# Kernel tuning notes

Measured on AMD Instinct MI355X. Metric: run time of the kernel, lower is better.

Reference implementation:

```python
import jax, jax.numpy as jnp
import numpy as np

B, C, H, W, NH = 4, 96, 256, 256, 4


def setup_inputs() -> dict:
    key = jax.random.key(0)
    ks = jax.random.split(key, 8)
    s = 0.05  # keep pre-activations well-scaled
    return {
        "x": jax.random.normal(ks[0], (B, C, H, W), jnp.float32),
        "ff": jax.random.normal(ks[1], (B, C, H, W), jnp.float32),
        "w_q": jax.random.normal(ks[2], (C, C, 1, 1), jnp.float32) * s,
        "w_kv": jax.random.normal(ks[3], (2 * C, C, 1, 1), jnp.float32) * s,
        "w_q_dw": jax.random.normal(ks[4], (C, 1, 3, 3), jnp.float32) * s,
        "w_kv_dw": jax.random.normal(ks[5], (2 * C, 1, 3, 3), jnp.float32) * s,
        "w_out": jax.random.normal(ks[6], (C, C, 1, 1), jnp.float32) * s,
        "temperature": jnp.ones((NH, 1, 1), jnp.float32),
    }


def _conv1x1(x, w):
    # pointwise conv == channel GEMM; w: [O, I, 1, 1]
    return jnp.einsum('bchw,oc->bohw', x, w[:, :, 0, 0])


def _dwconv3(x, w):
    # depthwise 3x3, padding=1; w: [C, 1, 3, 3]
    return jax.lax.conv_general_dilated(
        x, w, window_strides=(1, 1), padding='SAME',
        feature_group_count=x.shape[1],
        dimension_numbers=('NCHW', 'OIHW', 'NCHW'))


def _l2norm(t, eps=1e-12):
    # L2-normalize along last (HW) axis, torch F.normalize semantics
    n = jnp.sqrt(jnp.sum(t * t, axis=-1, keepdims=True))
    return t / jnp.maximum(n, eps)


def reference(x, ff, w_q, w_kv, w_q_dw, w_kv_dw, w_out, temperature):
    b, c, h, w = x.shape
    q = _dwconv3(_conv1x1(ff, w_q), w_q_dw)          # [B,C,H,W]
    kv = _dwconv3(_conv1x1(x, w_kv), w_kv_dw)        # [B,2C,H,W]
    k, v = jnp.split(kv, 2, axis=1)

    def heads(t):
        return t.reshape(b, NH, c // NH, h * w)       # [B,nh,c,HW]

    q = _l2norm(heads(q))
    k = _l2norm(heads(k))
    v = heads(v)
    # channel-wise (transposed) attention: [B,nh,c,c]
    attn = jax.nn.softmax(jnp.einsum('bhcn,bhdn->bhcd', q, k) * temperature, axis=-1)
    o = jnp.einsum('bhcd,bhdn->bhcn', attn, v).reshape(b, c, h, w)
    return _conv1x1(o, w_out)
```

## Files before the change

### kernel.cpp

```cpp
#include <hip/hip_runtime.h>
#include <hip/hip_bf16.h>
#include <hip/hip_fp16.h>

typedef unsigned int u32;
typedef unsigned short u16;
typedef _Float16 f16;

static constexpr int HWn = 65536;

typedef __attribute__((ext_vector_type(8))) f16 f16x8;
typedef __attribute__((ext_vector_type(2))) f16 f16x2;
typedef __attribute__((ext_vector_type(4))) float f32x4;

__device__ __forceinline__ float h2f(u16 u) {
    union { u16 s; f16 h; } z; z.s = u; return (float)z.h;
}
__device__ __forceinline__ u16 f2h(float f) {
    union { u16 s; f16 h; } z; z.h = (f16)f; return z.s;
}
__device__ __forceinline__ u32 pack2h(float a, float b) {
    union { u32 i; f16 h[2]; } z; z.h[0] = (f16)a; z.h[1] = (f16)b; return z.i;
}
__device__ __forceinline__ float hlo(u32 u) {
    union { u32 i; f16 h[2]; } z; z.i = u; return (float)z.h[0];
}
__device__ __forceinline__ float hhi(u32 u) {
    union { u32 i; f16 h[2]; } z; z.i = u; return (float)z.h[1];
}
__device__ __forceinline__ float sq2h(u32 a) {
    const float l = hlo(a), h = hhi(a);
    return fmaf(l, l, h * h);
}

#if defined(__has_builtin)
#if __has_builtin(__builtin_amdgcn_fdot2)
#define HAS_FDOT2 1
#endif
#endif
__device__ __forceinline__ float fdot2a(u32 a, u32 b, float c) {
#ifdef HAS_FDOT2
    union { u32 i; f16x2 h; } A, B; A.i = a; B.i = b;
    return __builtin_amdgcn_fdot2(A.h, B.h, c, false);
#else
    return fmaf(hlo(a), hlo(b), fmaf(hhi(a), hhi(b), c));
#endif
}

__device__ __forceinline__ int xoff(int px, int icb) {
    return px * 128 + (((icb ^ (px & 7) ^ ((px >> 3) & 7))) << 3);
}

__global__ __launch_bounds__(256) void k_prep_w(
    const float* __restrict__ wq, const float* __restrict__ wkv,
    u16* __restrict__ wf)
{
    const int i = blockIdx.x * 256 + threadIdx.x;
    if (i >= 288 * 96) return;
    const int row = i / 96, ic = i % 96;
    const float w = (row < 96) ? wq[row * 96 + ic] : wkv[(row - 96) * 96 + ic];
    wf[i] = f2h(w);
}

__global__ __launch_bounds__(256, 3) void k_conv_mfma(
    const float* __restrict__ ff, const float* __restrict__ x,
    const u16* __restrict__ wf,
    u16* __restrict__ qpre, u16* __restrict__ kvpre)
{
    const int b = blockIdx.z, sec = blockIdx.y;
    const int pxb = blockIdx.x * 256;
    const int tid = threadIdx.x;

    __shared__ __align__(16) u16 xs[16384];

    const float* src = (sec == 0 ? ff : x) + (size_t)b * 96 * HWn;
    const int icq = (tid >> 4) * 2;
    const int pxs = (tid & 15) * 8;
    const int lane = tid & 63;
    const int wv = tid >> 6;
    const int oc0 = (wv >> 1) * 48;
    const int pxw = (wv & 1) * 64;
    const int lr = lane & 15, lg = lane >> 4;

    float4 L[12];

    auto issue = [&](int px0) {
        #pragma unroll
        for (int p = 0; p < 3; ++p) {
            const float* rp0 = src + (size_t)(p * 32 + icq) * HWn + px0 + pxs;
            const float* rp1 = rp0 + HWn;
            L[p * 4 + 0] = *reinterpret_cast<const float4*>(rp0);
            L[p * 4 + 1] = *reinterpret_cast<const float4*>(rp0 + 4);
            L[p * 4 + 2] = *reinterpret_cast<const float4*>(rp1);
            L[p * 4 + 3] = *reinterpret_cast<const float4*>(rp1 + 4);
        }
    };
    auto stage = [&]() {
        #pragma unroll
        for (int p = 0; p < 3; ++p) {
            const int ic = p * 32 + icq;
            const int icb = ic >> 3, icl = ic & 7;
            const float e0[8] = {L[p*4+0].x, L[p*4+0].y, L[p*4+0].z, L[p*4+0].w,
                                 L[p*4+1].x, L[p*4+1].y, L[p*4+1].z, L[p*4+1].w};
            const float e1[8] = {L[p*4+2].x, L[p*4+2].y, L[p*4+2].z, L[p*4+2].w,
                                 L[p*4+3].x, L[p*4+3].y, L[p*4+3].z, L[p*4+3].w};
            #pragma unroll
            for (int j = 0; j < 8; ++j) {
                const int o = xoff(pxs + j, icb) + icl;
                *reinterpret_cast<u32*>(&xs[o]) = pack2h(e0[j], e1[j]);
            }
        }
    };
    auto compute = [&](int px0) {
        const int npass = (sec == 0) ? 1 : 2;
        #pragma unroll 1
        for (int kvs = 0; kvs < npass; ++kvs) {
            const u16* wh = wf + ((sec == 0) ? 0 : (96 + kvs * 96)) * 96;
            u16* dst = (sec == 0) ? (qpre + (size_t)b * 96 * HWn)
                                  : (kvpre + (size_t)b * 192 * HWn + (size_t)kvs * 96 * HWn);
            f32x4 acc[4][3];
            #pragma unroll
            for (int n = 0; n < 4; ++n)
                #pragma unroll
                for (int m = 0; m < 3; ++m)
                    acc[n][m] = (f32x4){0.f, 0.f, 0.f, 0.f};

            #pragma unroll 1
            for (int kt = 0; kt < 3; ++kt) {
                const int kb = kt * 32;
                f16x8 XA[4];
                #pragma unroll
                for (int n = 0; n < 4; ++n)
                    XA[n] = *(const f16x8*)(xs + xoff(pxw + n * 16 + lr, (kb >> 3) + lg));
                f16x8 WB[3];
                #pragma unroll
                for (int m = 0; m < 3; ++m)
                    WB[m] = *(const f16x8*)(wh + (oc0 + m * 16 + lr) * 96 + kb + lg * 8);
                #pragma unroll
                for (int n = 0; n < 4; ++n)
                    #pragma unroll
                    for (int m = 0; m < 3; ++m)
                        acc[n][m] = __builtin_amdgcn_mfma_f32_16x16x32_f16(XA[n], WB[m], acc[n][m], 0, 0, 0);
            }

            #pragma unroll
            for (int n = 0; n < 4; ++n) {
                #pragma unroll
                for (int m = 0; m < 3; ++m) {
                    const int oc = oc0 + m * 16 + lr;
                    ushort4 sv;
                    sv.x = f2h(acc[n][m][0]); sv.y = f2h(acc[n][m][1]);
                    sv.z = f2h(acc[n][m][2]); sv.w = f2h(acc[n][m][3]);
                    *reinterpret_cast<ushort4*>(dst + (size_t)oc * HWn + px0 + pxw + n * 16 + lg * 4) = sv;
                }
            }
        }
    };

    issue(pxb);
    stage();
    __syncthreads();
    issue(pxb + 128);
    compute(pxb);
    __syncthreads();
    stage();
    __syncthreads();
    compute(pxb + 128);
}

__device__ __forceinline__ void row3tap(
    const uint4 m, u32 lv, u32 rv, u32 w01, u32 w2z, float* a)
{
    const u32 P0 = m.x, P1 = m.y, P2 = m.z, P3 = m.w;
    const u32 s0 = (lv >> 16) | (P0 << 16);
    const u32 s1 = (P0 >> 16) | (P1 << 16);
    const u32 s2 = (P1 >> 16) | (P2 << 16);
    const u32 s3 = (P2 >> 16) | (P3 << 16);
    const u32 s4 = (P3 >> 16) | (rv << 16);
    a[0] = fdot2a(w2z, s1, fdot2a(w01, s0, a[0]));
    a[1] = fdot2a(w2z, P1, fdot2a(w01, P0, a[1]));
    a[2] = fdot2a(w2z, s2, fdot2a(w01, s1, a[2]));
    a[3] = fdot2a(w2z, P2, fdot2a(w01, P1, a[3]));
    a[4] = fdot2a(w2z, s3, fdot2a(w01, s2, a[4]));
    a[5] = fdot2a(w2z, P3, fdot2a(w01, P2, a[5]));
    a[6] = fdot2a(w2z, s4, fdot2a(w01, s3, a[6]));
    a[7] = fdot2a(w2z, rv, fdot2a(w01, P3, a[7]));
}

__global__ __launch_bounds__(512) void k_dw_qk(
    const u16* __restrict__ qpre, const u16* __restrict__ kvpre,
    const float* __restrict__ wqdw, const float* __restrict__ wkvdw,
    float* __restrict__ ssq, float* __restrict__ Sg)
{
    const int bid = blockIdx.x;
    const int wg = (bid & 7) * 256 + (bid >> 3);
    const int b = wg >> 9;
    const int rem = wg & 511;
    const int y = rem >> 1;
    const int tx = (rem & 1) * 128;
    const int tid = threadIdx.x;
    const int lane = tid & 63;
    const int pq = tid >> 4;
    const int chunk = tid & 15;
    const int x0l = chunk * 8;
    const int xg = tx + x0l;

    const bool vr0 = (y > 0), vr2 = (y < 255);
    const bool le = (chunk == 0) && (xg > 0);
    const bool re = (chunk == 15) && (xg + 8 < 256);

    __shared__ __align__(16) u16 qs[96][136];
    __shared__ __align__(16) u16 ks[96][136];

    auto addr = [&](int it, const u16*& src, const float*& wp, int& c, int& seg) {
        const int p = it * 32 + pq;
        if (p < 96) { c = p;      src = qpre  + ((size_t)(b * 96 + c)) * HWn;  wp = wqdw  + c * 9; seg = 0; }
        else        { c = p - 96; src = kvpre + ((size_t)(b * 192 + c)) * HWn; wp = wkvdw + c * 9; seg = 1; }
    };
    auto issue = [&](const u16* src, uint4* m, u32* el, u32* er) {
        const uint4 z = make_uint4(0u, 0u, 0u, 0u);
        const u16* r0 = src + (y - 1) * 256 + xg;
        const u16* r1 = r0 + 256;
        const u16* r2 = r1 + 256;
        m[0] = vr0 ? *reinterpret_cast<const uint4*>(r0) : z;
        m[1] = *reinterpret_cast<const uint4*>(r1);
        m[2] = vr2 ? *reinterpret_cast<const uint4*>(r2) : z;
        el[0] = (le && vr0) ? ((u32)r0[-1] << 16) : 0u;  er[0] = (re && vr0) ? (u32)r0[8] : 0u;
        el[1] = le ? ((u32)r1[-1] << 16) : 0u;           er[1] = re ? (u32)r1[8] : 0u;
        el[2] = (le && vr2) ? ((u32)r2[-1] << 16) : 0u;  er[2] = (re && vr2) ? (u32)r2[8] : 0u;
    };

    const u16* srcC; const float* wpC; int cC, segC;
    addr(0, srcC, wpC, cC, segC);
    uint4 mcur[3]; u32 elc[3], erc[3];
    issue(srcC, mcur, elc, erc);

    #pragma unroll 1
    for (int it = 0; it < 6; ++it) {
        const u16* srcN; const float* wpN; int cN, segN;
        uint4 mnx[3]; u32 eln[3], ern[3];
        if (it < 5) {
            addr(it + 1, srcN, wpN, cN, segN);
            issue(srcN, mnx, eln, ern);
        }

        float a[8] = {0.f, 0.f, 0.f, 0.f, 0.f, 0.f, 0.f, 0.f};
        #pragma unroll
        for (int r = 0; r < 3; ++r) {
            const u32 w01 = pack2h(wpC[r * 3 + 0], wpC[r * 3 + 1]);
            const u32 w2z = pack2h(wpC[r * 3 + 2], 0.f);
            const u32 lvn = __shfl((int)mcur[r].w, (lane - 1) & 63);
            const u32 rvn = __shfl((int)mcur[r].x, (lane + 1) & 63);
            const u32 lv = (chunk == 0)  ? elc[r] : lvn;
            const u32 rv = (chunk == 15) ? erc[r] : rvn;
            row3tap(mcur[r], lv, rv, w01, w2z, a);
        }

        const uint4 o = make_uint4(pack2h(a[0], a[1]), pack2h(a[2], a[3]),
                                   pack2h(a[4], a[5]), pack2h(a[6], a[7]));
        if (segC == 0) *reinterpret_cast<uint4*>(&qs[cC][x0l]) = o;
        else           *reinterpret_cast<uint4*>(&ks[cC][x0l]) = o;

        if (it < 5) {
            #pragma unroll
            for (int r = 0; r < 3; ++r) { mcur[r] = mnx[r]; elc[r] = eln[r]; erc[r] = ern[r]; }
            wpC = wpN; cC = cN; segC = segN;
        }
    }
    __syncthreads();

    if (tid < 384) {
        const int half = tid >= 192;
        const int r = tid - half * 192;
        const uint4* rr = reinterpret_cast<const uint4*>(
            (r < 96 ? &qs[r][0] : &ks[r - 96][0]) + half * 64);
        float s = 0.f;
        #pragma unroll
        for (int pch = 0; pch < 8; ++pch) {
            const uint4 a = rr[pch];
            s += sq2h(a.x) + sq2h(a.y) + sq2h(a.z) + sq2h(a.w);
        }
        atomicAdd(ssq + b * 192 + r, s);
    }

    {
        const int w = tid >> 6;
        const int h = w & 3, mt = w >> 2;
        const int lr2 = lane & 15, lg2 = lane >> 4;
        const int ar = h * 24 + min(mt * 16 + lr2, 23);
        f32x4 acc2[2];
        acc2[0] = (f32x4){0.f, 0.f, 0.f, 0.f};
        acc2[1] = (f32x4){0.f, 0.f, 0.f, 0.f};
        #pragma unroll
        for (int ks4 = 0; ks4 < 4; ++ks4) {
            const f16x8 A = *(const f16x8*)(&qs[ar][ks4 * 32 + lg2 * 8]);
            #pragma unroll
            for (int nt = 0; nt < 2; ++nt) {
                const int bc = h * 24 + min(nt * 16 + lr2, 23);
                const f16x8 B = *(const f16x8*)(&ks[bc][ks4 * 32 + lg2 * 8]);
                acc2[nt] = __builtin_amdgcn_mfma_f32_16x16x32_f16(A, B, acc2[nt], 0, 0, 0);
            }
        }
        #pragma unroll
        for (int nt = 0; nt < 2; ++nt) {
            const int col = nt * 16 + lr2;
            #pragma unroll
            for (int reg = 0; reg < 4; ++reg) {
                const int row24 = mt * 16 + lg2 * 4 + reg;
                if (row24 < 24 && col < 24)
                    atomicAdd(Sg + b * 2304 + h * 576 + row24 * 24 + col, acc2[nt][reg]);
            }
        }
    }
}

__global__ __launch_bounds__(256) void k_attn_fold(
    const float* __restrict__ ssq, const float* __restrict__ S,
    const float* __restrict__ temp, const float* __restrict__ w_out,
    u16* __restrict__ mf)
{
    const int b = blockIdx.x;
    const int tid = threadIdx.x;
    __shared__ float rq[96], rk[96], att[2304];

    if (tid < 96) {
        rq[tid] = 1.f / fmaxf(sqrtf(ssq[b * 192 + tid]), 1e-12f);
    } else if (tid < 192) {
        const int c = tid - 96;
        rk[c] = 1.f / fmaxf(sqrtf(ssq[b * 192 + 96 + c]), 1e-12f);
    }
    __syncthreads();

    if (tid < 96) {
        const int h = tid / 24, i = tid % 24;
        const float tmp = temp[h];
        const float rqi = rq[h * 24 + i];
        float l[24];
        float m = -1e30f;
        #pragma unroll
        for (int j = 0; j < 24; ++j) {
            l[j] = S[b * 2304 + (h * 24 + i) * 24 + j] * rqi * rk[h * 24 + j] * tmp;
            m = fmaxf(m, l[j]);
        }
        float ssum = 0.f;
        #pragma unroll
        for (int j = 0; j < 24; ++j) { l[j] = expf(l[j] - m); ssum += l[j]; }
        const float inv = 1.f / ssum;
        #pragma unroll
        for (int j = 0; j < 24; ++j) att[(h * 24 + i) * 24 + j] = l[j] * inv;
    }
    __syncthreads();

    for (int k = 0; k < 36; ++k) {
        const int id = k * 256 + tid;
        const int dg = id / 96, oc = id % 96;
        const int h = dg / 24, d24 = dg % 24;
        float s = 0.f;
        #pragma unroll
        for (int i = 0; i < 24; ++i) {
            s += w_out[oc * 96 + h * 24 + i] * att[(h * 24 + i) * 24 + d24];
        }
        mf[b * 9216 + oc * 96 + dg] = f2h(s);
    }
}

__global__ __launch_bounds__(256, 4) void k_v_out(
    const u16* __restrict__ kvpre, const float* __restrict__ wkvdw,
    const u16* __restrict__ mf, float* __restrict__ out)
{
    const int bid = blockIdx.x;
    const int wg = (bid & 7) * 256 + (bid >> 3);
    const int b = wg >> 9;
    const int rem = wg & 511;
    const int y = rem >> 1;
    const int tx = (rem & 1) * 128;
    const int tid = threadIdx.x;
    const int lane = tid & 63;
    const int slot = tid >> 4;
    const int chunk = tid & 15;
    const int x0l = chunk * 8;
    const int xg = tx + x0l;

    const bool vr0 = (y > 0), vr2 = (y < 255);
    const bool le = (chunk == 0) && (xg > 0);
    const bool re = (chunk == 15) && (xg + 8 < 256);

    __shared__ __align__(16) u16 xt[16384];

    auto issue = [&](int it, uint4* m0, uint4* m1, u32* e0l, u32* e0r, u32* e1l, u32* e1r) {
        const int dg = (it * 16 + slot) * 2;
        const u16* s0 = kvpre + ((size_t)(b * 192 + 96 + dg)) * HWn + (y - 1) * 256 + xg;
        const u16* s1 = s0 + HWn;
        const uint4 z = make_uint4(0u, 0u, 0u, 0u);
        m0[0] = vr0 ? *reinterpret_cast<const uint4*>(s0)       : z;
        m0[1] =       *reinterpret_cast<const uint4*>(s0 + 256);
        m0[2] = vr2 ? *reinterpret_cast<const uint4*>(s0 + 512) : z;
        m1[0] = vr0 ? *reinterpret_cast<const uint4*>(s1)       : z;
        m1[1] =       *reinterpret_cast<const uint4*>(s1 + 256);
        m1[2] = vr2 ? *reinterpret_cast<const uint4*>(s1 + 512) : z;
        e0l[0] = (le && vr0) ? ((u32)s0[-1] << 16) : 0u;   e0r[0] = (re && vr0) ? (u32)s0[8] : 0u;
        e0l[1] = le ? ((u32)s0[255] << 16) : 0u;           e0r[1] = re ? (u32)s0[264] : 0u;
        e0l[2] = (le && vr2) ? ((u32)s0[511] << 16) : 0u;  e0r[2] = (re && vr2) ? (u32)s0[520] : 0u;
        e1l[0] = (le && vr0) ? ((u32)s1[-1] << 16) : 0u;   e1r[0] = (re && vr0) ? (u32)s1[8] : 0u;
        e1l[1] = le ? ((u32)s1[255] << 16) : 0u;           e1r[1] = re ? (u32)s1[264] : 0u;
        e1l[2] = (le && vr2) ? ((u32)s1[511] << 16) : 0u;  e1r[2] = (re && vr2) ? (u32)s1[520] : 0u;
    };

    uint4 m0c[3], m1c[3]; u32 e0lc[3], e0rc[3], e1lc[3], e1rc[3];
    issue(0, m0c, m1c, e0lc, e0rc, e1lc, e1rc);

    #pragma unroll 1
    for (int it = 0; it < 3; ++it) {
        uint4 m0n[3], m1n[3]; u32 e0ln[3], e0rn[3], e1ln[3], e1rn[3];
        if (it < 2) issue(it + 1, m0n, m1n, e0ln, e0rn, e1ln, e1rn);

        const int dg = (it * 16 + slot) * 2;
        const float* wp0 = wkvdw + (96 + dg) * 9;
        const float* wp1 = wp0 + 9;

        float a0[8] = {0.f, 0.f, 0.f, 0.f, 0.f, 0.f, 0.f, 0.f};
        float a1[8] = {0.f, 0.f, 0.f, 0.f, 0.f, 0.f, 0.f, 0.f};
        #pragma unroll
        for (int r = 0; r < 3; ++r) {
            {
                const u32 w01 = pack2h(wp0[r * 3 + 0], wp0[r * 3 + 1]);
                const u32 w2z = pack2h(wp0[r * 3 + 2], 0.f);
                const u32 lvn = __shfl((int)m0c[r].w, (lane - 1) & 63);
                const u32 rvn = __shfl((int)m0c[r].x, (lane + 1) & 63);
                const u32 lv = (chunk == 0)  ? e0lc[r] : lvn;
                const u32 rv = (chunk == 15) ? e0rc[r] : rvn;
                row3tap(m0c[r], lv, rv, w01, w2z, a0);
            }
            {
                const u32 w01 = pack2h(wp1[r * 3 + 0], wp1[r * 3 + 1]);
                const u32 w2z = pack2h(wp1[r * 3 + 2], 0.f);
                const u32 lvn = __shfl((int)m1c[r].w, (lane - 1) & 63);
                const u32 rvn = __shfl((int)m1c[r].x, (lane + 1) & 63);
                const u32 lv = (chunk == 0)  ? e1lc[r] : lvn;
                const u32 rv = (chunk == 15) ? e1rc[r] : rvn;
                row3tap(m1c[r], lv, rv, w01, w2z, a1);
            }
        }

        const int icb = dg >> 3, icl = dg & 7;
        #pragma unroll
        for (int j = 0; j < 8; ++j) {
            *reinterpret_cast<u32*>(&xt[xoff(x0l + j, icb) + icl]) = pack2h(a0[j], a1[j]);
        }

        if (it < 2) {
            #pragma unroll
            for (int r = 0; r < 3; ++r) {
                m0c[r] = m0n[r]; m1c[r] = m1n[r];
                e0lc[r] = e0ln[r]; e0rc[r] = e0rn[r];
                e1lc[r] = e1ln[r]; e1rc[r] = e1rn[r];
            }
        }
    }
    __syncthreads();

    const u16* mh = mf + b * 9216;
    const int wv = tid >> 6;
    const int oc0 = (wv >> 1) * 48;
    const int pxw = (wv & 1) * 64;
    const int lr = lane & 15, lg = lane >> 4;

    f32x4 acc[4][3];
    #pragma unroll
    for (int n = 0; n < 4; ++n)
        #pragma unroll
        for (int m = 0; m < 3; ++m)
            acc[n][m] = (f32x4){0.f, 0.f, 0.f, 0.f};

    #pragma unroll 1
    for (int kt = 0; kt < 3; ++kt) {
        const int kb = kt * 32;
        f16x8 XA[4];
        #pragma unroll
        for (int n = 0; n < 4; ++n)
            XA[n] = *(const f16x8*)(xt + xoff(pxw + n * 16 + lr, (kb >> 3) + lg));
        f16x8 WB[3];
        #pragma unroll
        for (int m = 0; m < 3; ++m)
            WB[m] = *(const f16x8*)(mh + (oc0 + m * 16 + lr) * 96 + kb + lg * 8);
        #pragma unroll
        for (int n = 0; n < 4; ++n)
            #pragma unroll
            for (int m = 0; m < 3; ++m)
                acc[n][m] = __builtin_amdgcn_mfma_f32_16x16x32_f16(XA[n], WB[m], acc[n][m], 0, 0, 0);
    }

    #pragma unroll
    for (int n = 0; n < 4; ++n) {
        #pragma unroll
        for (int m = 0; m < 3; ++m) {
            const int oc = oc0 + m * 16 + lr;
            float* drow = out + ((size_t)(b * 96 + oc)) * HWn + y * 256 + tx;
            const float4 o4 = make_float4(acc[n][m][0], acc[n][m][1], acc[n][m][2], acc[n][m][3]);
            *reinterpret_cast<float4*>(drow + pxw + n * 16 + lg * 4) = o4;
        }
    }
}

extern "C" void kernel_launch(void* const* d_in, const int* in_sizes, int n_in,
                              void* d_out, int out_size, void* d_ws, size_t ws_size,
                              hipStream_t stream) {
    (void)in_sizes; (void)n_in; (void)out_size; (void)ws_size;
    const float* x      = (const float*)d_in[0];
    const float* ff     = (const float*)d_in[1];
    const float* w_q    = (const float*)d_in[2];
    const float* w_kv   = (const float*)d_in[3];
    const float* w_q_dw = (const float*)d_in[4];
    const float* w_kv_dw= (const float*)d_in[5];
    const float* w_out  = (const float*)d_in[6];
    const float* temp   = (const float*)d_in[7];
    float* out = (float*)d_out;

    char* ws = (char*)d_ws;
    u16* qpre   = (u16*)(ws);
    u16* kvpre  = (u16*)(ws + 50331648);
    float* ssq  = (float*)(ws + 150994944);
    float* S    = (float*)(ws + 150998016);
    u16* wf     = (u16*)(ws + 151034880);
    u16* mf     = (u16*)(ws + 151090176);

    hipMemsetAsync(ws + 150994944, 0, 3072 + 36864, stream);

    k_prep_w<<<108, 256, 0, stream>>>(w_q, w_kv, wf);
    k_conv_mfma<<<dim3(256, 2, 4), 256, 0, stream>>>(ff, x, wf, qpre, kvpre);
    k_dw_qk<<<dim3(2048), 512, 0, stream>>>(qpre, kvpre, w_q_dw, w_kv_dw, ssq, S);
    k_attn_fold<<<4, 256, 0, stream>>>(ssq, S, temp, w_out, mf);
    k_v_out<<<dim3(2048), 256, 0, stream>>>(kvpre, w_kv_dw, mf, out);
}
```

Baseline: 271.5 us.

## Store conv intermediates row-interleaved across all 288 channels per image row

```diff
diff --git a/kernel.cpp b/kernel.cpp
--- a/kernel.cpp
+++ b/kernel.cpp
@@ -7,6 +7,7 @@
 typedef _Float16 f16;
 
 static constexpr int HWn = 65536;
+static constexpr int RS = 288 * 256;
 
 typedef __attribute__((ext_vector_type(8))) f16 f16x8;
 typedef __attribute__((ext_vector_type(2))) f16 f16x2;
@@ -63,16 +64,17 @@
 
 __global__ __launch_bounds__(256, 3) void k_conv_mfma(
     const float* __restrict__ ff, const float* __restrict__ x,
-    const u16* __restrict__ wf,
-    u16* __restrict__ qpre, u16* __restrict__ kvpre)
+    const u16* __restrict__ wf, u16* __restrict__ ikv)
 {
     const int b = blockIdx.z, sec = blockIdx.y;
-    const int pxb = blockIdx.x * 256;
+    const int y = blockIdx.x;
     const int tid = threadIdx.x;
 
     __shared__ __align__(16) u16 xs[16384];
 
-    const float* src = (sec == 0 ? ff : x) + (size_t)b * 96 * HWn;
+    const float* src = (sec == 0 ? ff : x) + (size_t)b * 96 * HWn + y * 256;
+    u16* rowbase = ikv + (((size_t)b * 256 + y) * 288) * 256;
+
     const int icq = (tid >> 4) * 2;
     const int pxs = (tid & 15) * 8;
     const int lane = tid & 63;
@@ -83,10 +85,10 @@
 
     float4 L[12];
 
-    auto issue = [&](int px0) {
+    auto issue = [&](int x0) {
         #pragma unroll
         for (int p = 0; p < 3; ++p) {
-            const float* rp0 = src + (size_t)(p * 32 + icq) * HWn + px0 + pxs;
+            const float* rp0 = src + (size_t)(p * 32 + icq) * HWn + x0 + pxs;
             const float* rp1 = rp0 + HWn;
             L[p * 4 + 0] = *reinterpret_cast<const float4*>(rp0);
             L[p * 4 + 1] = *reinterpret_cast<const float4*>(rp0 + 4);
@@ -110,61 +112,60 @@
             }
         }
     };
-    auto compute = [&](int px0) {
+    auto compute = [&](int x0) {
         const int npass = (sec == 0) ? 1 : 2;
         #pragma unroll 1
         for (int kvs = 0; kvs < npass; ++kvs) {
-            const u16* wh = wf + ((sec == 0) ? 0 : (96 + kvs * 96)) * 96;
-            u16* dst = (sec == 0) ? (qpre + (size_t)b * 96 * HWn)
-                                  : (kvpre + (size_t)b * 192 * HWn + (size_t)kvs * 96 * HWn);
-            f32x4 acc[4][3];
-            #pragma unroll
-            for (int n = 0; n < 4; ++n)
+            const int pb = (sec == 0) ? 0 : (96 + kvs * 96);
+            const u16* wh = wf + pb * 96;
+            f32x4 acc[3][4];
+            #pragma unroll
+            for (int m = 0; m < 3; ++m)
                 #pragma unroll
-                for (int m = 0; m < 3; ++m)
-                    acc[n][m] = (f32x4){0.f, 0.f, 0.f, 0.f};
+                for (int n = 0; n < 4; ++n)
+                    acc[m][n] = (f32x4){0.f, 0.f, 0.f, 0.f};
 
             #pragma unroll 1
             for (int kt = 0; kt < 3; ++kt) {
                 const int kb = kt * 32;
-                f16x8 XA[4];
+                f16x8 B[4];
                 #pragma unroll
                 for (int n = 0; n < 4; ++n)
-                    XA[n] = *(const f16x8*)(xs + xoff(pxw + n * 16 + lr, (kb >> 3) + lg));
-                f16x8 WB[3];
+                    B[n] = *(const f16x8*)(xs + xoff(pxw + n * 16 + lr, (kb >> 3) + lg));
+                f16x8 A[3];
                 #pragma unroll
                 for (int m = 0; m < 3; ++m)
-                    WB[m] = *(const f16x8*)(wh + (oc0 + m * 16 + lr) * 96 + kb + lg * 8);
+                    A[m] = *(const f16x8*)(wh + (oc0 + m * 16 + lr) * 96 + kb + lg * 8);
                 #pragma unroll
-                for (int n = 0; n < 4; ++n)
+                for (int m = 0; m < 3; ++m)
                     #pragma unroll
-                    for (int m = 0; m < 3; ++m)
-                        acc[n][m] = __builtin_amdgcn_mfma_f32_16x16x32_f16(XA[n], WB[m], acc[n][m], 0, 0, 0);
-            }
-
-            #pragma unroll
-            for (int n = 0; n < 4; ++n) {
+                    for (int n = 0; n < 4; ++n)
+                        acc[m][n] = __builtin_amdgcn_mfma_f32_16x16x32_f16(A[m], B[n], acc[m][n], 0, 0, 0);
+            }
+
+            #pragma unroll
+            for (int m = 0; m < 3; ++m) {
                 #pragma unroll
-                for (int m = 0; m < 3; ++m) {
-                    const int oc = oc0 + m * 16 + lr;
-                    ushort4 sv;
-                    sv.x = f2h(acc[n][m][0]); sv.y = f2h(acc[n][m][1]);
-                    sv.z = f2h(acc[n][m][2]); sv.w = f2h(acc[n][m][3]);
-                    *reinterpret_cast<ushort4*>(dst + (size_t)oc * HWn + px0 + pxw + n * 16 + lg * 4) = sv;
+                for (int i = 0; i < 4; ++i) {
+                    const int oc = oc0 + m * 16 + lg * 4 + i;
+                    u16* drow = rowbase + (size_t)(pb + oc) * 256;
+                    #pragma unroll
+                    for (int n = 0; n < 4; ++n)
+                        drow[x0 + pxw + n * 16 + lr] = f2h(acc[m][n][i]);
                 }
             }
         }
     };
 
-    issue(pxb);
+    issue(0);
     stage();
     __syncthreads();
-    issue(pxb + 128);
-    compute(pxb);
+    issue(128);
+    compute(0);
     __syncthreads();
     stage();
     __syncthreads();
-    compute(pxb + 128);
+    compute(128);
 }
 
 __device__ __forceinline__ void row3tap(
@@ -187,7 +188,7 @@
 }
 
 __global__ __launch_bounds__(512) void k_dw_qk(
-    const u16* __restrict__ qpre, const u16* __restrict__ kvpre,
+    const u16* __restrict__ ikv,
     const float* __restrict__ wqdw, const float* __restrict__ wkvdw,
     float* __restrict__ ssq, float* __restrict__ Sg)
 {
@@ -211,16 +212,18 @@
     __shared__ __align__(16) u16 qs[96][136];
     __shared__ __align__(16) u16 ks[96][136];
 
-    auto addr = [&](int it, const u16*& src, const float*& wp, int& c, int& seg) {
+    const u16* rowm1 = ikv + (((size_t)b * 256 + (y - 1)) * 288) * 256;
+
+    auto addr = [&](int it, const u16*& r0, const float*& wp, int& c, int& seg) {
         const int p = it * 32 + pq;
-        if (p < 96) { c = p;      src = qpre  + ((size_t)(b * 96 + c)) * HWn;  wp = wqdw  + c * 9; seg = 0; }
-        else        { c = p - 96; src = kvpre + ((size_t)(b * 192 + c)) * HWn; wp = wkvdw + c * 9; seg = 1; }
+        r0 = rowm1 + (size_t)p * 256 + xg;
+        if (p < 96) { c = p;      wp = wqdw  + p * 9;        seg = 0; }
+        else        { c = p - 96; wp = wkvdw + (p - 96) * 9; seg = 1; }
     };
-    auto issue = [&](const u16* src, uint4* m, u32* el, u32* er) {
+    auto issue = [&](const u16* r0, uint4* m, u32* el, u32* er) {
         const uint4 z = make_uint4(0u, 0u, 0u, 0u);
-        const u16* r0 = src + (y - 1) * 256 + xg;
-        const u16* r1 = r0 + 256;
-        const u16* r2 = r1 + 256;
+        const u16* r1 = r0 + RS;
+        const u16* r2 = r1 + RS;
         m[0] = vr0 ? *reinterpret_cast<const uint4*>(r0) : z;
         m[1] = *reinterpret_cast<const uint4*>(r1);
         m[2] = vr2 ? *reinterpret_cast<const uint4*>(r2) : z;
@@ -364,7 +367,7 @@
 }
 
 __global__ __launch_bounds__(256, 4) void k_v_out(
-    const u16* __restrict__ kvpre, const float* __restrict__ wkvdw,
+    const u16* __restrict__ ikv, const float* __restrict__ wkvdw,
     const u16* __restrict__ mf, float* __restrict__ out)
 {
     const int bid = blockIdx.x;
@@ -386,23 +389,26 @@
 
     __shared__ __align__(16) u16 xt[16384];
 
+    const u16* rowm1 = ikv + (((size_t)b * 256 + (y - 1)) * 288) * 256;
+
     auto issue = [&](int it, uint4* m0, uint4* m1, u32* e0l, u32* e0r, u32* e1l, u32* e1r) {
         const int dg = (it * 16 + slot) * 2;
-        const u16* s0 = kvpre + ((size_t)(b * 192 + 96 + dg)) * HWn + (y - 1) * 256 + xg;
-        const u16* s1 = s0 + HWn;
+        const u16* r0 = rowm1 + (size_t)(192 + dg) * 256 + xg;
+        const u16* r1 = r0 + RS;
+        const u16* r2 = r1 + RS;
         const uint4 z = make_uint4(0u, 0u, 0u, 0u);
-        m0[0] = vr0 ? *reinterpret_cast<const uint4*>(s0)       : z;
-        m0[1] =       *reinterpret_cast<const uint4*>(s0 + 256);
-        m0[2] = vr2 ? *reinterpret_cast<const uint4*>(s0 + 512) : z;
-        m1[0] = vr0 ? *reinterpret_cast<const uint4*>(s1)       : z;
-        m1[1] =       *reinterpret_cast<const uint4*>(s1 + 256);
-        m1[2] = vr2 ? *reinterpret_cast<const uint4*>(s1 + 512) : z;
-        e0l[0] = (le && vr0) ? ((u32)s0[-1] << 16) : 0u;   e0r[0] = (re && vr0) ? (u32)s0[8] : 0u;
-        e0l[1] = le ? ((u32)s0[255] << 16) : 0u;           e0r[1] = re ? (u32)s0[264] : 0u;
-        e0l[2] = (le && vr2) ? ((u32)s0[511] << 16) : 0u;  e0r[2] = (re && vr2) ? (u32)s0[520] : 0u;
-        e1l[0] = (le && vr0) ? ((u32)s1[-1] << 16) : 0u;   e1r[0] = (re && vr0) ? (u32)s1[8] : 0u;
-        e1l[1] = le ? ((u32)s1[255] << 16) : 0u;           e1r[1] = re ? (u32)s1[264] : 0u;
-        e1l[2] = (le && vr2) ? ((u32)s1[511] << 16) : 0u;  e1r[2] = (re && vr2) ? (u32)s1[520] : 0u;
+        m0[0] = vr0 ? *reinterpret_cast<const uint4*>(r0) : z;
+        m0[1] =       *reinterpret_cast<const uint4*>(r1);
+        m0[2] = vr2 ? *reinterpret_cast<const uint4*>(r2) : z;
+        m1[0] = vr0 ? *reinterpret_cast<const uint4*>(r0 + 256) : z;
+        m1[1] =       *reinterpret_cast<const uint4*>(r1 + 256);
+        m1[2] = vr2 ? *reinterpret_cast<const uint4*>(r2 + 256) : z;
+        e0l[0] = (le && vr0) ? ((u32)r0[-1] << 16) : 0u;   e0r[0] = (re && vr0) ? (u32)r0[8] : 0u;
+        e0l[1] = le ? ((u32)r1[-1] << 16) : 0u;            e0r[1] = re ? (u32)r1[8] : 0u;
+        e0l[2] = (le && vr2) ? ((u32)r2[-1] << 16) : 0u;   e0r[2] = (re && vr2) ? (u32)r2[8] : 0u;
+        e1l[0] = (le && vr0) ? ((u32)r0[255] << 16) : 0u;  e1r[0] = (re && vr0) ? (u32)r0[264] : 0u;
+        e1l[1] = le ? ((u32)r1[255] << 16) : 0u;           e1r[1] = re ? (u32)r1[264] : 0u;
+        e1l[2] = (le && vr2) ? ((u32)r2[255] << 16) : 0u;  e1r[2] = (re && vr2) ? (u32)r2[264] : 0u;
     };
 
     uint4 m0c[3], m1c[3]; u32 e0lc[3], e0rc[3], e1lc[3], e1rc[3];
@@ -516,8 +522,7 @@
     float* out = (float*)d_out;
 
     char* ws = (char*)d_ws;
-    u16* qpre   = (u16*)(ws);
-    u16* kvpre  = (u16*)(ws + 50331648);
+    u16* ikv    = (u16*)(ws);
     float* ssq  = (float*)(ws + 150994944);
     float* S    = (float*)(ws + 150998016);
     u16* wf     = (u16*)(ws + 151034880);
@@ -526,8 +531,8 @@
     hipMemsetAsync(ws + 150994944, 0, 3072 + 36864, stream);
 
     k_prep_w<<<108, 256, 0, stream>>>(w_q, w_kv, wf);
-    k_conv_mfma<<<dim3(256, 2, 4), 256, 0, stream>>>(ff, x, wf, qpre, kvpre);
-    k_dw_qk<<<dim3(2048), 512, 0, stream>>>(qpre, kvpre, w_q_dw, w_kv_dw, ssq, S);
+    k_conv_mfma<<<dim3(256, 2, 4), 256, 0, stream>>>(ff, x, wf, ikv);
+    k_dw_qk<<<dim3(2048), 512, 0, stream>>>(ikv, w_q_dw, w_kv_dw, ssq, S);
     k_attn_fold<<<4, 256, 0, stream>>>(ssq, S, temp, w_out, mf);
-    k_v_out<<<dim3(2048), 256, 0, stream>>>(kvpre, w_kv_dw, mf, out);
-}
+    k_v_out<<<dim3(2048), 256, 0, stream>>>(ikv, w_kv_dw, mf, out);
+}
```

After: 265.4 us. -2.3%, faster.
